# Performance work log

Measured on AMD Instinct MI355X. Metric: run time of the kernel, lower is better.

The kernel has to match this reference:

```python
import jax, jax.numpy as jnp
import numpy as np

IN_F, OUT_F = 4096, 11008
IN_G, OUT_G = 8, 1
NUM_CB, CB_SIZE = 2, 256


def setup_inputs() -> dict:
    key = jax.random.key(0)
    k1, k2, k3, k4, k5 = jax.random.split(key, 5)
    no, ni = OUT_F // OUT_G, IN_F // IN_G
    x = jax.random.normal(k1, (4, 2048, IN_F), dtype=jnp.float32)
    codes = jax.random.randint(k2, (no, ni, NUM_CB), 0, CB_SIZE, dtype=jnp.int32)
    codebooks = jax.random.normal(k3, (NUM_CB, CB_SIZE, OUT_G, IN_G), dtype=jnp.float32)
    scales = jax.random.uniform(k4, (no, 1, 1, 1), dtype=jnp.float32) + 0.5
    bias = jax.random.normal(k5, (OUT_F,), dtype=jnp.float32)
    return {"x": x, "codes": codes, "codebooks": codebooks, "scales": scales, "bias": bias}


def _dequantize_weight(codes, codebooks, scales):
    # codes: [no, ni, M] ints; codebooks: [M, C, og, ig]; scales: [no, 1, 1, 1]
    M = codebooks.shape[0]
    og, ig = codebooks.shape[2], codebooks.shape[3]
    no, ni = codes.shape[0], codes.shape[1]
    # gather each codebook's entry and sum over codebooks -> [no, ni, og, ig]
    m_idx = jnp.arange(M)[None, None, :]
    gathered = codebooks[m_idx, codes]            # [no, ni, M, og, ig]
    deq = gathered.sum(axis=2) * scales           # [no, ni, og, ig]
    # reorder groups back to dense weight [out_features, in_features]
    return deq.transpose(0, 2, 1, 3).reshape(no * og, ni * ig)


def reference(x, codes, codebooks, scales, bias):
    w = _dequantize_weight(codes, codebooks, scales)  # [OUT_F, IN_F]
    return jnp.einsum("bsi,oi->bso", x, w) + bias
```

## Files before the change

### kernel.cpp

```cpp
#include <hip/hip_runtime.h>
#include <hip/hip_bf16.h>
#include <stdint.h>

#define IN_F   4096
#define OUT_F  11008
#define M_TOK  8192

typedef __attribute__((ext_vector_type(4))) int   int32x4;
typedef __attribute__((ext_vector_type(4))) float f32x4;

__device__ __forceinline__ float block_rowmax(float m, float* red, int t) {
    red[t] = m; __syncthreads();
    for (int s = 128; s > 0; s >>= 1) {
        if (t < s) red[t] = fmaxf(red[t], red[t + s]);
        __syncthreads();
    }
    float r = red[0]; __syncthreads();
    return fmaxf(r, 1e-8f);
}

__global__ __launch_bounds__(256) void k_qx(
        const float* __restrict__ x, signed char* __restrict__ Xq,
        float* __restrict__ sx) {
    __shared__ float red[256];
    int r = blockIdx.x, t = threadIdx.x;
    const float4* xr = (const float4*)(x + (size_t)r * IN_F) + t * 4;
    float4 v0 = xr[0], v1 = xr[1], v2 = xr[2], v3 = xr[3];
    float m = 0.f;
#define MX4(v) m = fmaxf(m, fmaxf(fmaxf(fabsf(v.x), fabsf(v.y)), fmaxf(fabsf(v.z), fabsf(v.w))))
    MX4(v0); MX4(v1); MX4(v2); MX4(v3);
    float rm = block_rowmax(m, red, t);
    if (t == 0) sx[r] = rm / 127.f;
    float inv = 127.f / rm;
    union { signed char c[16]; uint4 u; } pk;
#define Q4(v, o) pk.c[o] = (signed char)__float2int_rn(v.x * inv);            \
                 pk.c[o+1] = (signed char)__float2int_rn(v.y * inv);          \
                 pk.c[o+2] = (signed char)__float2int_rn(v.z * inv);          \
                 pk.c[o+3] = (signed char)__float2int_rn(v.w * inv)
    Q4(v0, 0); Q4(v1, 4); Q4(v2, 8); Q4(v3, 12);
    *(uint4*)(Xq + (size_t)r * IN_F + t * 16) = pk.u;
}

__global__ __launch_bounds__(256) void k_qw(
        const int* __restrict__ codes,
        const float* __restrict__ codebooks,
        const float* __restrict__ scales,
        signed char* __restrict__ Wq, float* __restrict__ sw) {
    __shared__ float cb[4096];
    __shared__ float red[256];
    int o = blockIdx.x, t = threadIdx.x;
    {
        const float4* cbg = (const float4*)codebooks;
        float4* cbl = (float4*)cb;
#pragma unroll
        for (int i = 0; i < 4; ++i) cbl[t + i * 256] = cbg[t + i * 256];
    }
    __syncthreads();
    const int2* cp = (const int2*)codes + (size_t)o * 512 + t * 2;
    int2 c0 = cp[0], c1 = cp[1];
    float e[16]; float m = 0.f;
#pragma unroll
    for (int j = 0; j < 8; ++j) {
        e[j]     = cb[c0.x * 8 + j] + cb[2048 + c0.y * 8 + j];
        e[8 + j] = cb[c1.x * 8 + j] + cb[2048 + c1.y * 8 + j];
    }
#pragma unroll
    for (int j = 0; j < 16; ++j) m = fmaxf(m, fabsf(e[j]));
    float rm = block_rowmax(m, red, t);
    if (t == 0) sw[o] = scales[o] * rm / 127.f;
    float inv = 127.f / rm;
    union { signed char c[16]; uint4 u; } pk;
#pragma unroll
    for (int j = 0; j < 16; ++j) pk.c[j] = (signed char)__float2int_rn(e[j] * inv);
    *(uint4*)(Wq + (size_t)o * IN_F + t * 16) = pk.u;
}


#define BARRIER() __builtin_amdgcn_s_barrier()
#define VMW(n)    asm volatile("s_waitcnt vmcnt(" #n ")")

#define GL16(gp, lp) __builtin_amdgcn_global_load_lds(                        \
    (const __attribute__((address_space(1))) void*)(gp),                      \
    (__attribute__((address_space(3))) void*)(lp), 16, 0, 0)

__global__ __launch_bounds__(512, 2) void k_gemm(
        const signed char* __restrict__ A,
        const signed char* __restrict__ B,
        const float* __restrict__ sx,
        const float* __restrict__ sw,
        const float* __restrict__ bias,
        float* __restrict__ out) {
    __shared__ signed char lA0[256 * 128];
    __shared__ signed char lA1[256 * 128];
    __shared__ signed char lB0[256 * 128];
    __shared__ signed char lB1[256 * 128];

    const int tid = threadIdx.x;
    const int l = tid & 63;
    const int w = tid >> 6;
    const int wm = w >> 2, wn = w & 3;

    int lid = blockIdx.x;
    int xcd = lid & 7, j = lid >> 3;
    int bx = j >> 2;
    int by = (xcd << 2) + (j & 3);
    const int rowBase = by * 256;
    const int colBase = bx * 256;

    const int srow = w * 8 + (l >> 3);
    const int scol = ((l & 7) ^ ((l >> 3) & 7)) << 4;
    const signed char* gA = A + (size_t)(rowBase + srow) * IN_F + scol;
    const signed char* gB = B + (size_t)(colBase + srow) * IN_F + scol;
    signed char* lA0w = &lA0[w * 8 * 128];
    signed char* lA1w = &lA1[w * 8 * 128];
    signed char* lB0w = &lB0[w * 8 * 128];
    signed char* lB1w = &lB1[w * 8 * 128];

#define STAGEQ_(P, t, q) do {                                                 \
    const signed char* _g = (((q) < 2) ? gA : gB) + (size_t)(t) * 128;        \
    signed char* _l = (((q) < 2) ? lA##P##w : lB##P##w);                      \
    const int _r = ((q) & 1) * 128;                                           \
    GL16(_g + (size_t)_r * IN_F,        _l + _r * 128);                       \
    GL16(_g + (size_t)(_r + 64) * IN_F, _l + (_r + 64) * 128);                \
} while (0)

    const int frow = l & 15, g = l >> 4;
    const int cho0 = ((g ^ (frow & 7)) << 4);
    const int cho1 = (((4 + g) ^ (frow & 7)) << 4);
    const char* rowA0 = (const char*)&lA0[(wm * 128 + frow) * 128];
    const char* rowA1 = (const char*)&lA1[(wm * 128 + frow) * 128];
    const char* rowB0 = (const char*)&lB0[(wn * 64 + frow) * 128];
    const char* rowB1 = (const char*)&lB1[(wn * 64 + frow) * 128];
#define LDA_(P, m, kk) (*(const int32x4*)(rowA##P + (m) * 2048 + ((kk) ? cho1 : cho0)))
#define LDB_(P, n, kk) (*(const int32x4*)(rowB##P + (n) * 2048 + ((kk) ? cho1 : cho0)))

    int32x4 acc[8][4] = {};
    int32x4 ar[4][2], br[4][2];

#define QUAD(M0, N0) do {                                                     \
    __builtin_amdgcn_s_setprio(1);                                            \
    _Pragma("unroll") for (int mm = 0; mm < 4; ++mm)                          \
    _Pragma("unroll") for (int nn = 0; nn < 2; ++nn)                          \
    _Pragma("unroll") for (int kk = 0; kk < 2; ++kk)                          \
        acc[(M0) + mm][(N0) + nn] = __builtin_amdgcn_mfma_i32_16x16x64_i8(    \
            ar[mm][kk], br[(N0) + nn][kk], acc[(M0) + mm][(N0) + nn], 0, 0, 0);\
    __builtin_amdgcn_s_setprio(0);                                            \
} while (0)

#define RD_A03_B01(P) do {                                                    \
    _Pragma("unroll") for (int mm = 0; mm < 4; ++mm) {                        \
        ar[mm][0] = LDA_(P, mm, 0); ar[mm][1] = LDA_(P, mm, 1); }             \
    br[0][0] = LDB_(P, 0, 0); br[0][1] = LDB_(P, 0, 1);                       \
    br[1][0] = LDB_(P, 1, 0); br[1][1] = LDB_(P, 1, 1);                       \
} while (0)
#define RD_B23(P) do {                                                        \
    br[2][0] = LDB_(P, 2, 0); br[2][1] = LDB_(P, 2, 1);                       \
    br[3][0] = LDB_(P, 3, 0); br[3][1] = LDB_(P, 3, 1);                       \
} while (0)
#define RD_A47(P) do {                                                        \
    _Pragma("unroll") for (int mm = 0; mm < 4; ++mm) {                        \
        ar[mm][0] = LDA_(P, 4 + mm, 0); ar[mm][1] = LDA_(P, 4 + mm, 1); }     \
} while (0)

    STAGEQ_(0, 0, 0); STAGEQ_(0, 0, 1); STAGEQ_(0, 0, 2); STAGEQ_(0, 0, 3);
    STAGEQ_(1, 1, 2); STAGEQ_(1, 1, 3); STAGEQ_(1, 1, 0); STAGEQ_(1, 1, 1);
    VMW(8); BARRIER();

    for (int i = 0; i < 15; ++i) {
        int t = 2 * i;
        RD_A03_B01(0);
        QUAD(0, 0); BARRIER();
        RD_B23(0);
        QUAD(0, 2); BARRIER();
        RD_A47(0); STAGEQ_(0, t + 2, 2); STAGEQ_(0, t + 2, 3);
        QUAD(4, 2); BARRIER();
        STAGEQ_(0, t + 2, 0); STAGEQ_(0, t + 2, 1); VMW(8);
        QUAD(4, 0); BARRIER();
        RD_A03_B01(1);
        QUAD(0, 0); BARRIER();
        RD_B23(1);
        QUAD(0, 2); BARRIER();
        RD_A47(1); STAGEQ_(1, t + 3, 2); STAGEQ_(1, t + 3, 3);
        QUAD(4, 2); BARRIER();
        STAGEQ_(1, t + 3, 0); STAGEQ_(1, t + 3, 1); VMW(8);
        QUAD(4, 0); BARRIER();
    }

    RD_A03_B01(0);
    QUAD(0, 0); BARRIER();
    RD_B23(0);
    QUAD(0, 2); BARRIER();
    RD_A47(0);
    QUAD(4, 2); BARRIER();
    VMW(0);
    QUAD(4, 0); BARRIER();
    RD_A03_B01(1);
    QUAD(0, 0); BARRIER();
    RD_B23(1);
    QUAD(0, 2); BARRIER();
    RD_A47(1);
    QUAD(4, 2); BARRIER();
    QUAD(4, 0);

#pragma unroll
    for (int n = 0; n < 4; ++n) {
        int gcol = colBase + wn * 64 + n * 16 + frow;
        float swv = sw[gcol];
        float bv = bias[gcol];
#pragma unroll
        for (int m = 0; m < 8; ++m) {
            int grow0 = rowBase + wm * 128 + m * 16 + g * 4;
            float4 sx4 = *(const float4*)&sx[grow0];
            out[(size_t)(grow0 + 0) * OUT_F + gcol] = (float)acc[m][n][0] * sx4.x * swv + bv;
            out[(size_t)(grow0 + 1) * OUT_F + gcol] = (float)acc[m][n][1] * sx4.y * swv + bv;
            out[(size_t)(grow0 + 2) * OUT_F + gcol] = (float)acc[m][n][2] * sx4.z * swv + bv;
            out[(size_t)(grow0 + 3) * OUT_F + gcol] = (float)acc[m][n][3] * sx4.w * swv + bv;
        }
    }
}

extern "C" void kernel_launch(void* const* d_in, const int* in_sizes, int n_in,
                              void* d_out, int out_size, void* d_ws, size_t ws_size,
                              hipStream_t stream) {
    const float* x         = (const float*)d_in[0];
    const int*   codes     = (const int*)d_in[1];
    const float* codebooks = (const float*)d_in[2];
    const float* scales    = (const float*)d_in[3];
    const float* bias      = (const float*)d_in[4];
    float* out = (float*)d_out;

    signed char* Wq = (signed char*)d_ws;
    signed char* Xq = Wq + (size_t)OUT_F * IN_F;
    float* sx = (float*)(Xq + (size_t)M_TOK * IN_F);
    float* sw = sx + M_TOK;

    k_qx<<<M_TOK, 256, 0, stream>>>(x, Xq, sx);
    k_qw<<<OUT_F, 256, 0, stream>>>(codes, codebooks, scales, Wq, sw);
    k_gemm<<<1376, 512, 0, stream>>>(Xq, Wq, sx, sw, bias, out);
}
```

Before: 466.0 us.

## Restructure int8 GEMM main loop to halve barriers and stagger tile staging

Reworks the software-pipelined main loop of the int8 GEMM so each half-iteration uses two barriers instead of four. The staging of the next K tile is split across phases so that loads for the other buffer are issued while the current one is computed, with a shallower vmcnt wait. This targets barrier stalls and exposed global-load latency, but it relies on the new staging order leaving LDS buffers free before they are overwritten. A mistake in that order would cause a race or corrupt results.

```diff
diff --git a/kernel.cpp b/kernel.cpp
--- a/kernel.cpp
+++ b/kernel.cpp
@@ -7,7 +7,6 @@
 #define M_TOK  8192
 
 typedef __attribute__((ext_vector_type(4))) int   int32x4;
-typedef __attribute__((ext_vector_type(4))) float f32x4;
 
 __device__ __forceinline__ float block_rowmax(float m, float* red, int t) {
     red[t] = m; __syncthreads();
@@ -163,44 +162,48 @@
 } while (0)
 
     STAGEQ_(0, 0, 0); STAGEQ_(0, 0, 1); STAGEQ_(0, 0, 2); STAGEQ_(0, 0, 3);
-    STAGEQ_(1, 1, 2); STAGEQ_(1, 1, 3); STAGEQ_(1, 1, 0); STAGEQ_(1, 1, 1);
-    VMW(8); BARRIER();
+    STAGEQ_(1, 1, 2); STAGEQ_(1, 1, 3);
+    VMW(4); BARRIER();
 
     for (int i = 0; i < 15; ++i) {
-        int t = 2 * i;
+        int e = 2 * i, o = 2 * i + 1;
         RD_A03_B01(0);
-        QUAD(0, 0); BARRIER();
+        STAGEQ_(1, o, 0); STAGEQ_(1, o, 1);
+        QUAD(0, 0);
         RD_B23(0);
-        QUAD(0, 2); BARRIER();
-        RD_A47(0); STAGEQ_(0, t + 2, 2); STAGEQ_(0, t + 2, 3);
-        QUAD(4, 2); BARRIER();
-        STAGEQ_(0, t + 2, 0); STAGEQ_(0, t + 2, 1); VMW(8);
-        QUAD(4, 0); BARRIER();
+        QUAD(0, 2);
+        BARRIER();
+        RD_A47(0);
+        STAGEQ_(0, e + 2, 2); STAGEQ_(0, e + 2, 3);
+        QUAD(4, 2); QUAD(4, 0);
+        VMW(4); BARRIER();
         RD_A03_B01(1);
-        QUAD(0, 0); BARRIER();
+        STAGEQ_(0, e + 2, 0); STAGEQ_(0, e + 2, 1);
+        QUAD(0, 0);
         RD_B23(1);
-        QUAD(0, 2); BARRIER();
-        RD_A47(1); STAGEQ_(1, t + 3, 2); STAGEQ_(1, t + 3, 3);
-        QUAD(4, 2); BARRIER();
-        STAGEQ_(1, t + 3, 0); STAGEQ_(1, t + 3, 1); VMW(8);
-        QUAD(4, 0); BARRIER();
+        QUAD(0, 2);
+        BARRIER();
+        RD_A47(1);
+        STAGEQ_(1, o + 2, 2); STAGEQ_(1, o + 2, 3);
+        QUAD(4, 2); QUAD(4, 0);
+        VMW(4); BARRIER();
     }
 
     RD_A03_B01(0);
-    QUAD(0, 0); BARRIER();
+    STAGEQ_(1, 31, 0); STAGEQ_(1, 31, 1);
+    QUAD(0, 0);
     RD_B23(0);
-    QUAD(0, 2); BARRIER();
+    QUAD(0, 2);
+    BARRIER();
     RD_A47(0);
-    QUAD(4, 2); BARRIER();
-    VMW(0);
-    QUAD(4, 0); BARRIER();
+    QUAD(4, 2); QUAD(4, 0);
+    VMW(0); BARRIER();
     RD_A03_B01(1);
-    QUAD(0, 0); BARRIER();
+    QUAD(0, 0);
     RD_B23(1);
-    QUAD(0, 2); BARRIER();
+    QUAD(0, 2);
     RD_A47(1);
-    QUAD(4, 2); BARRIER();
-    QUAD(4, 0);
+    QUAD(4, 2); QUAD(4, 0);
 
 #pragma unroll
     for (int n = 0; n < 4; ++n) {
```

New measurement: 470.8 us. Within noise of the previous version (+1.0%).
